# Performance work log

Hardware: AMD Instinct MI355X
Metric: run time of the kernel (lower is better)

## Reference

```python
import jax, jax.numpy as jnp
import numpy as np

B, Q, D, T, S = 64, 1024, 256, 64, 3  # batch, queries, hidden_dim, targets/image, max_steps


def _hat(w):
    # (...,3) -> (...,3,3)
    z = jnp.zeros_like(w[..., 0])
    wx, wy, wz = w[..., 0], w[..., 1], w[..., 2]
    return jnp.stack([
        jnp.stack([z, -wz, wy], -1),
        jnp.stack([wz, z, -wx], -1),
        jnp.stack([-wy, wx, z], -1),
    ], -2)


def _vee(W):
    return jnp.stack([W[..., 2, 1] - W[..., 1, 2],
                      W[..., 0, 2] - W[..., 2, 0],
                      W[..., 1, 0] - W[..., 0, 1]], -1) * 0.5


def exp_SO3(omega):
    # Rodrigues: (...,3) -> (...,3,3)
    theta = jnp.clip(jnp.linalg.norm(omega, axis=-1, keepdims=True), 1e-12, None)  # (...,1)
    K = _hat(omega / theta)
    K2 = K @ K
    I = jnp.eye(3, dtype=omega.dtype)
    st = jnp.sin(theta)[..., None]
    ct = jnp.cos(theta)[..., None]
    R = I + st * K + (1.0 - ct) * K2
    Ho = _hat(omega)
    R_small = I + Ho + 0.5 * (Ho @ Ho)
    small = (theta[..., 0] < 1e-5).astype(omega.dtype)[..., None, None]
    return R * (1.0 - small) + R_small * small


def log_SO3(R):
    # (...,3,3) -> (...,3)
    tr = jnp.clip(R[..., 0, 0] + R[..., 1, 1] + R[..., 2, 2], -1.0, 3.0)
    theta = jnp.arccos(jnp.clip((tr - 1.0) * 0.5, -1.0, 1.0))[..., None]  # (...,1)
    W = 0.5 * (R - jnp.swapaxes(R, -1, -2))
    v = _vee(W)
    w = v / jnp.clip(jnp.sin(theta), 1e-12, None) * theta
    small = (theta[..., 0] < 1e-5).astype(R.dtype)[..., None]
    return w * (1.0 - small) + v * small


def _mlp(x, w1, b1, w2, b2):
    # Linear -> ReLU -> Linear -> Sigmoid
    h = jax.nn.relu(x @ w1 + b1)
    return jax.nn.sigmoid(h @ w2 + b2)


def setup_inputs() -> dict:
    key = jax.random.key(0)
    ks = iter(jax.random.split(key, 32))

    def lin(fin, fout):
        bound = 1.0 / np.sqrt(fin)
        kw, kb = jax.random.split(next(ks))
        w = jax.random.uniform(kw, (fin, fout), jnp.float32, -bound, bound)
        b = jax.random.uniform(kb, (fout,), jnp.float32, -bound, bound)
        return w, b

    R_pred = exp_SO3(0.5 * jax.random.normal(next(ks), (B, Q, 3), jnp.float32))
    t_pred = jax.random.normal(next(ks), (B, Q, 3), jnp.float32)
    pred_boxes = jax.random.uniform(next(ks), (B, Q, 4), jnp.float32)
    query_features = jax.random.normal(next(ks), (B, Q, D), jnp.float32)
    tgt_R = exp_SO3(0.5 * jax.random.normal(next(ks), (B, T, 3), jnp.float32))
    tgt_t = jax.random.normal(next(ks), (B, T, 3), jnp.float32)
    tgt_boxes = jax.random.uniform(next(ks), (B, T, 4), jnp.float32)
    tgt_features = jax.random.normal(next(ks), (B, T, D), jnp.float32)

    sp_w1, sp_b1 = lin(D, D // 2); sp_w2, sp_b2 = lin(D // 2, S)
    rw_w1, rw_b1 = lin(D, D // 2); rw_w2, rw_b2 = lin(D // 2, 1)
    tw_w1, tw_b1 = lin(D, D // 2); tw_w2, tw_b2 = lin(D // 2, 1)
    mn_w1, mn_b1 = lin(2 * D, D);  mn_w2, mn_b2 = lin(D, 1)
    global_strength = jnp.float32(0.5)

    return dict(R_pred=R_pred, t_pred=t_pred, pred_boxes=pred_boxes,
                query_features=query_features, tgt_R=tgt_R, tgt_t=tgt_t,
                tgt_boxes=tgt_boxes, tgt_features=tgt_features,
                sp_w1=sp_w1, sp_b1=sp_b1, sp_w2=sp_w2, sp_b2=sp_b2,
                rw_w1=rw_w1, rw_b1=rw_b1, rw_w2=rw_w2, rw_b2=rw_b2,
                tw_w1=tw_w1, tw_b1=tw_b1, tw_w2=tw_w2, tw_b2=tw_b2,
                mn_w1=mn_w1, mn_b1=mn_b1, mn_w2=mn_w2, mn_b2=mn_b2,
                global_strength=global_strength)


def reference(R_pred, t_pred, pred_boxes, query_features, tgt_R, tgt_t,
              tgt_boxes, tgt_features, sp_w1, sp_b1, sp_w2, sp_b2,
              rw_w1, rw_b1, rw_w2, rw_b2, tw_w1, tw_b1, tw_w2, tw_b2,
              mn_w1, mn_b1, mn_w2, mn_b2, global_strength):
    # adaptive per-step scales: (B,S)
    step_scales = _mlp(query_features.mean(axis=1), sp_w1, sp_b1, sp_w2, sp_b2)
    step_scales = step_scales * jnp.clip(global_strength, 0.0, 1.0)
    rot_w = _mlp(query_features, rw_w1, rw_b1, rw_w2, rw_b2)    # (B,Q,1)
    trans_w = _mlp(query_features, tw_w1, tw_b1, tw_w2, tw_b2)  # (B,Q,1)

    # nearest-neighbor matching on box centers
    c_pred = pred_boxes[..., :2]               # (B,Q,2)
    cgt = tgt_boxes[..., :2]                   # (B,T,2)
    d = jnp.sum((c_pred[:, :, None, :] - cgt[:, None, :, :]) ** 2, -1)  # (B,Q,T)
    nn_idx = jnp.argmin(d, axis=-1)            # (B,Q)

    matched_feat = jnp.take_along_axis(tgt_features, nn_idx[..., None], axis=1)  # (B,Q,D)
    combined = jnp.concatenate([query_features, matched_feat], -1)               # (B,Q,2D)
    match_w = _mlp(combined, mn_w1, mn_b1, mn_w2, mn_b2)                          # (B,Q,1)

    Rmatch = jnp.take_along_axis(tgt_R, nn_idx[..., None, None], axis=1)  # (B,Q,3,3)
    tmatch = jnp.take_along_axis(tgt_t, nn_idx[..., None], axis=1)        # (B,Q,3)

    Rb, tb = R_pred, t_pred
    for s in range(S):
        scale = step_scales[:, s][:, None, None]                 # (B,1,1)
        w = log_SO3(jnp.swapaxes(Rb, -1, -2) @ Rmatch)           # (B,Q,3)
        adaptive_w = w * rot_w * match_w * scale
        Rb = Rb @ exp_SO3(adaptive_w)
        tb = tb + (tmatch - tb) * trans_w * match_w * scale
    return Rb, tb
```

## Files before the change

kernel.cpp:

```cpp
#include <hip/hip_runtime.h>

typedef __bf16 bf16;
typedef __bf16 bf16x8 __attribute__((ext_vector_type(8)));
typedef float  f32x4  __attribute__((ext_vector_type(4)));

#define QTOT 1024
#define DD   256

__global__ void k_prep(const float* __restrict__ wr, const float* __restrict__ wt,
                       const float* __restrict__ wm, const float* __restrict__ qf,
                       bf16* __restrict__ pk, float* __restrict__ wsMean2) {
  __shared__ float sPart[8][256];
  int blk = blockIdx.x;
  if (blk < 96) {
    int gid = blk * 256 + threadIdx.x;
    const float* W; int N, nK, idx; bf16* dst;
    if (gid < 4096)      { W = wr; N = 128; nK = 8;  idx = gid;        dst = pk; }
    else if (gid < 8192) { W = wt; N = 128; nK = 8;  idx = gid - 4096; dst = pk + 32768; }
    else                 { W = wm; N = 256; nK = 16; idx = gid - 8192; dst = pk + 65536; }
    int tile = idx >> 6, lane = idx & 63;
    int ni = tile / nK, ki = tile % nK;
    int l15 = lane & 15, quad = lane >> 4;
    int n = ni * 16 + l15;
    int kbase = ki * 32 + quad * 8;
    bf16x8 v;
#pragma unroll
    for (int j = 0; j < 8; ++j) v[j] = (bf16)W[(size_t)(kbase + j) * N + n];
    *(bf16x8*)(dst + (size_t)idx * 8) = v;
  } else {
    int mb = blk - 96;
    int b = mb >> 1, chunk = mb & 1;
    int tid = threadIdx.x;
    int rg = tid >> 5, c8 = tid & 31;
    float acc[8] = {0.f,0.f,0.f,0.f,0.f,0.f,0.f,0.f};
    const float* base = qf + ((size_t)b * QTOT + (size_t)chunk * 512) * DD + c8 * 8;
#pragma unroll 4
    for (int it = 0; it < 64; ++it) {
      f32x4 v0 = *(const f32x4*)(base + (size_t)(it * 8 + rg) * DD);
      f32x4 v1 = *(const f32x4*)(base + (size_t)(it * 8 + rg) * DD + 4);
#pragma unroll
      for (int j = 0; j < 4; ++j) { acc[j] += v0[j]; acc[4 + j] += v1[j]; }
    }
#pragma unroll
    for (int j = 0; j < 8; ++j) sPart[rg][c8 * 8 + j] = acc[j];
    __syncthreads();
    float s = 0.f;
#pragma unroll
    for (int g = 0; g < 8; ++g) s += sPart[g][tid];
    wsMean2[mb * 256 + tid] = s;
  }
}

__global__ void k_mid(const float* __restrict__ tgt_f, const bf16* __restrict__ pk,
                      const float* __restrict__ wsMean2,
                      const float* __restrict__ w1, const float* __restrict__ b1,
                      const float* __restrict__ w2, const float* __restrict__ b2,
                      const float* __restrict__ gs,
                      bf16* __restrict__ tgtp, float* __restrict__ outS) {
  __shared__ __align__(16) bf16 sT[64 * 264];
  __shared__ float sMean[256];
  __shared__ float sPart2[256];
  __shared__ float sHid[128];
  int blk = blockIdx.x, tid = threadIdx.x;
  if (blk < 64) {
    int b = blk;
    const float* srcT = tgt_f + ((size_t)b * 64) * DD;
#pragma unroll
    for (int it = 0; it < 8; ++it) {
      int idx = tid + it * 256;
      int row = idx >> 5, c8 = idx & 31;
      f32x4 t0 = *(const f32x4*)(srcT + (size_t)row * DD + c8 * 8);
      f32x4 t1 = *(const f32x4*)(srcT + (size_t)row * DD + c8 * 8 + 4);
      bf16x8 tv;
#pragma unroll
      for (int j = 0; j < 4; ++j) { tv[j] = (bf16)t0[j]; tv[4 + j] = (bf16)t1[j]; }
      *(bf16x8*)(sT + row * 264 + c8 * 8) = tv;
    }
    __syncthreads();
    const int lane = tid & 63, wv = tid >> 6;
    const int l15 = lane & 15, quad = lane >> 4, koff = quad * 8;
    const bf16x8* pMatch = (const bf16x8*)(pk + 65536);
    f32x4 acc[4][4];
#pragma unroll
    for (int mt = 0; mt < 4; ++mt)
#pragma unroll
      for (int nl = 0; nl < 4; ++nl) acc[mt][nl] = f32x4{0.f, 0.f, 0.f, 0.f};
#pragma unroll
    for (int ks = 0; ks < 8; ++ks) {
      bf16x8 A[4];
#pragma unroll
      for (int mt = 0; mt < 4; ++mt)
        A[mt] = *(const bf16x8*)(sT + (mt * 16 + l15) * 264 + ks * 32 + koff);
#pragma unroll
      for (int nl = 0; nl < 4; ++nl) {
        bf16x8 Bm = pMatch[((size_t)((4 * wv + nl) * 16 + 8 + ks)) * 64 + lane];
#pragma unroll
        for (int mt = 0; mt < 4; ++mt)
          acc[mt][nl] = __builtin_amdgcn_mfma_f32_16x16x32_bf16(A[mt], Bm, acc[mt][nl], 0, 0, 0);
      }
    }
    bf16* dst = tgtp + (size_t)b * 64 * 256;
#pragma unroll
    for (int mt = 0; mt < 4; ++mt)
#pragma unroll
      for (int nl = 0; nl < 4; ++nl) {
        int n = (4 * wv + nl) * 16 + l15;
#pragma unroll
        for (int i = 0; i < 4; ++i) {
          int t = mt * 16 + quad * 4 + i;
          dst[t * 256 + n] = (bf16)acc[mt][nl][i];
        }
      }
  } else {
    int b = blk - 64;
    sMean[tid] = (wsMean2[(2 * b) * 256 + tid] + wsMean2[(2 * b + 1) * 256 + tid]) * (1.f / 1024.f);
    __syncthreads();
    int hid = tid & 127, half = tid >> 7;
    float ph = 0.f;
#pragma unroll 8
    for (int dd = 0; dd < 128; ++dd) {
      int d = half * 128 + dd;
      ph += sMean[d] * w1[d * 128 + hid];
    }
    sPart2[tid] = ph;
    __syncthreads();
    if (tid < 128) sHid[tid] = fmaxf(sPart2[tid] + sPart2[tid + 128] + b1[tid], 0.f);
    __syncthreads();
    if (tid < 3) {
      float o = b2[tid];
      for (int k = 0; k < 128; ++k) o += sHid[k] * w2[k * 3 + tid];
      float g = fminf(fmaxf(gs[0], 0.f), 1.f);
      outS[b * 3 + tid] = g / (1.f + expf(-o));
    }
  }
}

__launch_bounds__(256, 4)
__global__ void k_main(const float* __restrict__ R_pred, const float* __restrict__ t_pred,
                       const float* __restrict__ pred_boxes, const float* __restrict__ qf,
                       const float* __restrict__ tgt_R, const float* __restrict__ tgt_t,
                       const float* __restrict__ tgt_boxes,
                       const float* __restrict__ rw_b1, const float* __restrict__ rw_w2, const float* __restrict__ rw_b2,
                       const float* __restrict__ tw_b1, const float* __restrict__ tw_w2, const float* __restrict__ tw_b2,
                       const float* __restrict__ mn_b1, const float* __restrict__ mn_w2, const float* __restrict__ mn_b2,
                       const bf16* __restrict__ pk, const bf16* __restrict__ tgtp,
                       const float* __restrict__ scales, float* __restrict__ out) {
  __shared__ __align__(16) bf16 sQ[64 * 264];
  __shared__ float sRedA[4][64];
  __shared__ float sRedB[4][64];
  __shared__ float sRedM[4][64];
  __shared__ int   sNN[64];

  const int tid = threadIdx.x;
  const int b  = blockIdx.x >> 4;
  const int qb = (blockIdx.x & 15) << 6;

  {
    const float* srcQ = qf + ((size_t)(b * QTOT + qb)) * DD;
#pragma unroll
    for (int it = 0; it < 8; ++it) {
      int idx = tid + it * 256;
      int row = idx >> 5, c8 = idx & 31;
      f32x4 q0 = *(const f32x4*)(srcQ + (size_t)row * DD + c8 * 8);
      f32x4 q1 = *(const f32x4*)(srcQ + (size_t)row * DD + c8 * 8 + 4);
      bf16x8 qv;
#pragma unroll
      for (int j = 0; j < 4; ++j) { qv[j] = (bf16)q0[j]; qv[4 + j] = (bf16)q1[j]; }
      *(bf16x8*)(sQ + row * 264 + c8 * 8) = qv;
    }
  }
  {
    int q = tid >> 2, ch = tid & 3;
    size_t gq = (size_t)(b * QTOT + qb + q);
    float px = pred_boxes[gq * 4 + 0];
    float py = pred_boxes[gq * 4 + 1];
    const float* tb = tgt_boxes + ((size_t)b * 64 + ch * 16) * 4;
    float best = 3.4e38f; int bi = ch * 16;
    for (int i = 0; i < 16; ++i) {
      f32x4 bx = *(const f32x4*)(tb + (size_t)i * 4);
      float dx = px - bx[0], dy = py - bx[1];
      float d = __fadd_rn(__fmul_rn(dx, dx), __fmul_rn(dy, dy));
      if (d < best) { best = d; bi = ch * 16 + i; }
    }
#pragma unroll
    for (int m = 1; m < 4; m <<= 1) {
      float pv = __shfl_xor(best, m);
      int   pi = __shfl_xor(bi, m);
      if (pv < best || (pv == best && pi < bi)) { best = pv; bi = pi; }
    }
    if ((tid & 3) == 0) sNN[q] = bi;
  }
  __syncthreads();

  const int lane = tid & 63, wv = tid >> 6;
  const int l15 = lane & 15, quad = lane >> 4;
  const int koff = quad * 8;
  const bf16x8* pRot   = (const bf16x8*)pk;
  const bf16x8* pTrans = (const bf16x8*)(pk + 32768);
  const bf16x8* pMatch = (const bf16x8*)(pk + 65536);

  {
    f32x4 accR[4][2];
#pragma unroll
    for (int mt = 0; mt < 4; ++mt)
#pragma unroll
      for (int nl = 0; nl < 2; ++nl) accR[mt][nl] = f32x4{0.f, 0.f, 0.f, 0.f};
#pragma unroll
    for (int ks = 0; ks < 8; ++ks) {
      bf16x8 A[4];
#pragma unroll
      for (int mt = 0; mt < 4; ++mt)
        A[mt] = *(const bf16x8*)(sQ + (mt * 16 + l15) * 264 + ks * 32 + koff);
#pragma unroll
      for (int nl = 0; nl < 2; ++nl) {
        bf16x8 Br = pRot[((size_t)((2 * wv + nl) * 8 + ks)) * 64 + lane];
#pragma unroll
        for (int mt = 0; mt < 4; ++mt)
          accR[mt][nl] = __builtin_amdgcn_mfma_f32_16x16x32_bf16(A[mt], Br, accR[mt][nl], 0, 0, 0);
      }
    }
    float b1r[2], w2r[2];
#pragma unroll
    for (int nl = 0; nl < 2; ++nl) {
      int n = (2 * wv + nl) * 16 + l15;
      b1r[nl] = rw_b1[n]; w2r[nl] = rw_w2[n];
    }
#pragma unroll
    for (int mt = 0; mt < 4; ++mt)
#pragma unroll
      for (int i = 0; i < 4; ++i) {
        float pr = 0.f;
#pragma unroll
        for (int nl = 0; nl < 2; ++nl) pr += fmaxf(accR[mt][nl][i] + b1r[nl], 0.f) * w2r[nl];
        pr += __shfl_xor(pr, 1); pr += __shfl_xor(pr, 2); pr += __shfl_xor(pr, 4); pr += __shfl_xor(pr, 8);
        if (l15 == 0) sRedA[wv][mt * 16 + quad * 4 + i] = pr;
      }
  }
  {
    f32x4 accT[4][2];
#pragma unroll
    for (int mt = 0; mt < 4; ++mt)
#pragma unroll
      for (int nl = 0; nl < 2; ++nl) accT[mt][nl] = f32x4{0.f, 0.f, 0.f, 0.f};
#pragma unroll
    for (int ks = 0; ks < 8; ++ks) {
      bf16x8 A[4];
#pragma unroll
      for (int mt = 0; mt < 4; ++mt)
        A[mt] = *(const bf16x8*)(sQ + (mt * 16 + l15) * 264 + ks * 32 + koff);
#pragma unroll
      for (int nl = 0; nl < 2; ++nl) {
        bf16x8 Bt = pTrans[((size_t)((2 * wv + nl) * 8 + ks)) * 64 + lane];
#pragma unroll
        for (int mt = 0; mt < 4; ++mt)
          accT[mt][nl] = __builtin_amdgcn_mfma_f32_16x16x32_bf16(A[mt], Bt, accT[mt][nl], 0, 0, 0);
      }
    }
    float b1t[2], w2t[2];
#pragma unroll
    for (int nl = 0; nl < 2; ++nl) {
      int n = (2 * wv + nl) * 16 + l15;
      b1t[nl] = tw_b1[n]; w2t[nl] = tw_w2[n];
    }
#pragma unroll
    for (int mt = 0; mt < 4; ++mt)
#pragma unroll
      for (int i = 0; i < 4; ++i) {
        float pt = 0.f;
#pragma unroll
        for (int nl = 0; nl < 2; ++nl) pt += fmaxf(accT[mt][nl][i] + b1t[nl], 0.f) * w2t[nl];
        pt += __shfl_xor(pt, 1); pt += __shfl_xor(pt, 2); pt += __shfl_xor(pt, 4); pt += __shfl_xor(pt, 8);
        if (l15 == 0) sRedB[wv][mt * 16 + quad * 4 + i] = pt;
      }
  }
  __syncthreads();

  float rw, tw;
  {
    int q = wv * 16 + l15;
    float vr = sRedA[0][q] + sRedA[1][q] + sRedA[2][q] + sRedA[3][q] + rw_b2[0];
    float vt = sRedB[0][q] + sRedB[1][q] + sRedB[2][q] + sRedB[3][q] + tw_b2[0];
    rw = 1.f / (1.f + expf(-vr));
    tw = 1.f / (1.f + expf(-vt));
  }

  {
    f32x4 accM[4][4];
#pragma unroll
    for (int mt = 0; mt < 4; ++mt)
#pragma unroll
      for (int nl = 0; nl < 4; ++nl) accM[mt][nl] = f32x4{0.f, 0.f, 0.f, 0.f};
#pragma unroll
    for (int ks = 0; ks < 8; ++ks) {
      bf16x8 A[4];
#pragma unroll
      for (int mt = 0; mt < 4; ++mt)
        A[mt] = *(const bf16x8*)(sQ + (mt * 16 + l15) * 264 + ks * 32 + koff);
#pragma unroll
      for (int nl = 0; nl < 4; ++nl) {
        bf16x8 Bm = pMatch[((size_t)((4 * wv + nl) * 16 + ks)) * 64 + lane];
#pragma unroll
        for (int mt = 0; mt < 4; ++mt)
          accM[mt][nl] = __builtin_amdgcn_mfma_f32_16x16x32_bf16(A[mt], Bm, accM[mt][nl], 0, 0, 0);
      }
    }
    float b1m[4], w2m[4];
#pragma unroll
    for (int nl = 0; nl < 4; ++nl) {
      int n = (4 * wv + nl) * 16 + l15;
      b1m[nl] = mn_b1[n]; w2m[nl] = mn_w2[n];
    }
    const bf16* tpb = tgtp + (size_t)b * 64 * 256;
#pragma unroll
    for (int mt = 0; mt < 4; ++mt)
#pragma unroll
      for (int i = 0; i < 4; ++i) {
        int nnq = sNN[mt * 16 + quad * 4 + i];
        const bf16* tprow = tpb + (size_t)nnq * 256;
        float pm = 0.f;
#pragma unroll
        for (int nl = 0; nl < 4; ++nl) {
          float tp = (float)tprow[(4 * wv + nl) * 16 + l15];
          pm += fmaxf(accM[mt][nl][i] + b1m[nl] + tp, 0.f) * w2m[nl];
        }
        pm += __shfl_xor(pm, 1); pm += __shfl_xor(pm, 2); pm += __shfl_xor(pm, 4); pm += __shfl_xor(pm, 8);
        if (l15 == 0) sRedM[wv][mt * 16 + quad * 4 + i] = pm;
      }
  }
  __syncthreads();

  if (quad == 0) {
    int q = wv * 16 + l15;
    float vm = sRedM[0][q] + sRedM[1][q] + sRedM[2][q] + sRedM[3][q] + mn_b2[0];
    float mw = 1.f / (1.f + expf(-vm));
    size_t gq = (size_t)(b * QTOT + qb + q);
    float R[9], Rm[9], t[3], tm[3];
#pragma unroll
    for (int i = 0; i < 9; ++i) R[i] = R_pred[gq * 9 + i];
#pragma unroll
    for (int c = 0; c < 3; ++c) t[c] = t_pred[gq * 3 + c];
    size_t gt = (size_t)b * 64 + sNN[q];
#pragma unroll
    for (int i = 0; i < 9; ++i) Rm[i] = tgt_R[gt * 9 + i];
#pragma unroll
    for (int c = 0; c < 3; ++c) tm[c] = tgt_t[gt * 3 + c];

    for (int s = 0; s < 3; ++s) {
      float sc = scales[b * 3 + s];
      float cr = rw * mw * sc, ctr = tw * mw * sc;
      float Ax[9];
#pragma unroll
      for (int i = 0; i < 3; ++i)
#pragma unroll
        for (int j = 0; j < 3; ++j)
          Ax[i * 3 + j] = R[0 + i] * Rm[0 + j] + R[3 + i] * Rm[3 + j] + R[6 + i] * Rm[6 + j];
      float tr = fminf(fmaxf(Ax[0] + Ax[4] + Ax[8], -1.f), 3.f);
      float cthe = fminf(fmaxf((tr - 1.f) * 0.5f, -1.f), 1.f);
      float th = acosf(cthe);
      float vx = 0.5f * (Ax[7] - Ax[5]);
      float vy = 0.5f * (Ax[2] - Ax[6]);
      float vz = 0.5f * (Ax[3] - Ax[1]);
      float f = (th < 1e-5f) ? 1.f : th / fmaxf(sinf(th), 1e-12f);
      float ax = vx * f * cr, ay = vy * f * cr, az = vz * f * cr;
      float th2 = ax * ax + ay * ay + az * az;
      float thn = sqrtf(th2);
      float E[9];
      if (thn < 1e-5f) {
        E[0] = 1.f + 0.5f * (ax * ax - th2); E[1] = -az + 0.5f * ax * ay;        E[2] =  ay + 0.5f * ax * az;
        E[3] =  az + 0.5f * ax * ay;         E[4] = 1.f + 0.5f * (ay * ay - th2); E[5] = -ax + 0.5f * ay * az;
        E[6] = -ay + 0.5f * ax * az;         E[7] =  ax + 0.5f * ay * az;         E[8] = 1.f + 0.5f * (az * az - th2);
      } else {
        float kx = ax / thn, ky = ay / thn, kz = az / thn;
        float st = sinf(thn), co = cosf(thn), c1 = 1.f - co;
        E[0] = co + c1 * kx * kx;      E[1] = c1 * kx * ky - st * kz; E[2] = c1 * kx * kz + st * ky;
        E[3] = c1 * kx * ky + st * kz; E[4] = co + c1 * ky * ky;      E[5] = c1 * ky * kz - st * kx;
        E[6] = c1 * kx * kz - st * ky; E[7] = c1 * ky * kz + st * kx; E[8] = co + c1 * kz * kz;
      }
      float Rn[9];
#pragma unroll
      for (int i = 0; i < 3; ++i)
#pragma unroll
        for (int j = 0; j < 3; ++j)
          Rn[i * 3 + j] = R[i * 3 + 0] * E[j] + R[i * 3 + 1] * E[3 + j] + R[i * 3 + 2] * E[6 + j];
#pragma unroll
      for (int i = 0; i < 9; ++i) R[i] = Rn[i];
#pragma unroll
      for (int c = 0; c < 3; ++c) t[c] += (tm[c] - t[c]) * ctr;
    }
#pragma unroll
    for (int i = 0; i < 9; ++i) out[gq * 9 + i] = R[i];
#pragma unroll
    for (int c = 0; c < 3; ++c) out[(size_t)589824 + gq * 3 + c] = t[c];
  }
}

extern "C" void kernel_launch(void* const* d_in, const int* in_sizes, int n_in,
                              void* d_out, int out_size, void* d_ws, size_t ws_size,
                              hipStream_t stream) {
  const float* R_pred     = (const float*)d_in[0];
  const float* t_pred     = (const float*)d_in[1];
  const float* pred_boxes = (const float*)d_in[2];
  const float* qf         = (const float*)d_in[3];
  const float* tgt_R      = (const float*)d_in[4];
  const float* tgt_t      = (const float*)d_in[5];
  const float* tgt_boxes  = (const float*)d_in[6];
  const float* tgt_f      = (const float*)d_in[7];
  const float* sp_w1 = (const float*)d_in[8];
  const float* sp_b1 = (const float*)d_in[9];
  const float* sp_w2 = (const float*)d_in[10];
  const float* sp_b2 = (const float*)d_in[11];
  const float* rw_w1 = (const float*)d_in[12];
  const float* rw_b1 = (const float*)d_in[13];
  const float* rw_w2 = (const float*)d_in[14];
  const float* rw_b2 = (const float*)d_in[15];
  const float* tw_w1 = (const float*)d_in[16];
  const float* tw_b1 = (const float*)d_in[17];
  const float* tw_w2 = (const float*)d_in[18];
  const float* tw_b2 = (const float*)d_in[19];
  const float* mn_w1 = (const float*)d_in[20];
  const float* mn_b1 = (const float*)d_in[21];
  const float* mn_w2 = (const float*)d_in[22];
  const float* mn_b2 = (const float*)d_in[23];
  const float* gs    = (const float*)d_in[24];

  float* wsScales = (float*)d_ws;
  float* wsMean2  = (float*)((char*)d_ws + 1024);
  bf16*  pk       = (bf16*)((char*)d_ws + 1024 + 131072);
  bf16*  tgtp     = (bf16*)((char*)d_ws + 1024 + 131072 + 393216);
  float* out      = (float*)d_out;

  k_prep<<<224, 256, 0, stream>>>(rw_w1, tw_w1, mn_w1, qf, pk, wsMean2);
  k_mid<<<128, 256, 0, stream>>>(tgt_f, pk, wsMean2, sp_w1, sp_b1, sp_w2, sp_b2, gs, tgtp, wsScales);
  k_main<<<1024, 256, 0, stream>>>(R_pred, t_pred, pred_boxes, qf, tgt_R, tgt_t, tgt_boxes,
                                   rw_b1, rw_w2, rw_b2, tw_b1, tw_w2, tw_b2, mn_b1, mn_w2, mn_b2,
                                   pk, tgtp, wsScales, out);
}
```

Before: 212.5 us.

## Give each wave its own 16 queries, keep A fragments in registers, drop LDS

Splits work so each wave owns 16 queries and computes all hidden units of the three MLPs for them, instead of all four waves splitting the hidden units of 64 shared queries. Query features are loaded from global straight into register A fragments, which removes the shared sQ tile, the cross-wave partial-sum reductions and the block-level barriers. In exchange, every wave now streams the full packed weight matrices, which multiplies weight loads per block by four. Register pressure also rises from holding eight A fragments.

```diff
diff --git a/kernel.cpp b/kernel.cpp
--- a/kernel.cpp
+++ b/kernel.cpp
@@ -145,33 +145,18 @@
                        const float* __restrict__ mn_b1, const float* __restrict__ mn_w2, const float* __restrict__ mn_b2,
                        const bf16* __restrict__ pk, const bf16* __restrict__ tgtp,
                        const float* __restrict__ scales, float* __restrict__ out) {
-  __shared__ __align__(16) bf16 sQ[64 * 264];
-  __shared__ float sRedA[4][64];
-  __shared__ float sRedB[4][64];
-  __shared__ float sRedM[4][64];
-  __shared__ int   sNN[64];
+  __shared__ float sRW[4][16], sTW[4][16], sMW[4][16];
+  __shared__ int   sNNw[4][16];
 
   const int tid = threadIdx.x;
+  const int lane = tid & 63, wv = tid >> 6;
+  const int l15 = lane & 15, quad = lane >> 4;
   const int b  = blockIdx.x >> 4;
-  const int qb = (blockIdx.x & 15) << 6;
-
-  {
-    const float* srcQ = qf + ((size_t)(b * QTOT + qb)) * DD;
-#pragma unroll
-    for (int it = 0; it < 8; ++it) {
-      int idx = tid + it * 256;
-      int row = idx >> 5, c8 = idx & 31;
-      f32x4 q0 = *(const f32x4*)(srcQ + (size_t)row * DD + c8 * 8);
-      f32x4 q1 = *(const f32x4*)(srcQ + (size_t)row * DD + c8 * 8 + 4);
-      bf16x8 qv;
-#pragma unroll
-      for (int j = 0; j < 4; ++j) { qv[j] = (bf16)q0[j]; qv[4 + j] = (bf16)q1[j]; }
-      *(bf16x8*)(sQ + row * 264 + c8 * 8) = qv;
-    }
-  }
-  {
-    int q = tid >> 2, ch = tid & 3;
-    size_t gq = (size_t)(b * QTOT + qb + q);
+  const int qw = ((blockIdx.x & 15) << 6) + wv * 16;
+
+  {
+    int q = lane >> 2, ch = lane & 3;
+    size_t gq = (size_t)(b * QTOT + qw + q);
     float px = pred_boxes[gq * 4 + 0];
     float py = pred_boxes[gq * 4 + 1];
     const float* tb = tgt_boxes + ((size_t)b * 64 + ch * 16) * 4;
@@ -188,158 +173,131 @@
       int   pi = __shfl_xor(bi, m);
       if (pv < best || (pv == best && pi < bi)) { best = pv; bi = pi; }
     }
-    if ((tid & 3) == 0) sNN[q] = bi;
-  }
-  __syncthreads();
-
-  const int lane = tid & 63, wv = tid >> 6;
-  const int l15 = lane & 15, quad = lane >> 4;
-  const int koff = quad * 8;
+    if (ch == 0) sNNw[wv][q] = bi;
+  }
+
+  bf16x8 Areg[8];
+  {
+    const float* rowp = qf + ((size_t)(b * QTOT + qw + l15)) * DD + quad * 8;
+#pragma unroll
+    for (int ks = 0; ks < 8; ++ks) {
+      f32x4 a0 = *(const f32x4*)(rowp + ks * 32);
+      f32x4 a1 = *(const f32x4*)(rowp + ks * 32 + 4);
+#pragma unroll
+      for (int j = 0; j < 4; ++j) { Areg[ks][j] = (bf16)a0[j]; Areg[ks][4 + j] = (bf16)a1[j]; }
+    }
+  }
+
   const bf16x8* pRot   = (const bf16x8*)pk;
   const bf16x8* pTrans = (const bf16x8*)(pk + 32768);
   const bf16x8* pMatch = (const bf16x8*)(pk + 65536);
 
   {
-    f32x4 accR[4][2];
-#pragma unroll
-    for (int mt = 0; mt < 4; ++mt)
-#pragma unroll
-      for (int nl = 0; nl < 2; ++nl) accR[mt][nl] = f32x4{0.f, 0.f, 0.f, 0.f};
-#pragma unroll
-    for (int ks = 0; ks < 8; ++ks) {
-      bf16x8 A[4];
-#pragma unroll
-      for (int mt = 0; mt < 4; ++mt)
-        A[mt] = *(const bf16x8*)(sQ + (mt * 16 + l15) * 264 + ks * 32 + koff);
-#pragma unroll
-      for (int nl = 0; nl < 2; ++nl) {
-        bf16x8 Br = pRot[((size_t)((2 * wv + nl) * 8 + ks)) * 64 + lane];
-#pragma unroll
-        for (int mt = 0; mt < 4; ++mt)
-          accR[mt][nl] = __builtin_amdgcn_mfma_f32_16x16x32_bf16(A[mt], Br, accR[mt][nl], 0, 0, 0);
-      }
-    }
-    float b1r[2], w2r[2];
-#pragma unroll
-    for (int nl = 0; nl < 2; ++nl) {
-      int n = (2 * wv + nl) * 16 + l15;
-      b1r[nl] = rw_b1[n]; w2r[nl] = rw_w2[n];
-    }
-#pragma unroll
-    for (int mt = 0; mt < 4; ++mt)
-#pragma unroll
-      for (int i = 0; i < 4; ++i) {
-        float pr = 0.f;
-#pragma unroll
-        for (int nl = 0; nl < 2; ++nl) pr += fmaxf(accR[mt][nl][i] + b1r[nl], 0.f) * w2r[nl];
-        pr += __shfl_xor(pr, 1); pr += __shfl_xor(pr, 2); pr += __shfl_xor(pr, 4); pr += __shfl_xor(pr, 8);
-        if (l15 == 0) sRedA[wv][mt * 16 + quad * 4 + i] = pr;
-      }
-  }
-  {
-    f32x4 accT[4][2];
-#pragma unroll
-    for (int mt = 0; mt < 4; ++mt)
-#pragma unroll
-      for (int nl = 0; nl < 2; ++nl) accT[mt][nl] = f32x4{0.f, 0.f, 0.f, 0.f};
-#pragma unroll
-    for (int ks = 0; ks < 8; ++ks) {
-      bf16x8 A[4];
-#pragma unroll
-      for (int mt = 0; mt < 4; ++mt)
-        A[mt] = *(const bf16x8*)(sQ + (mt * 16 + l15) * 264 + ks * 32 + koff);
-#pragma unroll
-      for (int nl = 0; nl < 2; ++nl) {
-        bf16x8 Bt = pTrans[((size_t)((2 * wv + nl) * 8 + ks)) * 64 + lane];
-#pragma unroll
-        for (int mt = 0; mt < 4; ++mt)
-          accT[mt][nl] = __builtin_amdgcn_mfma_f32_16x16x32_bf16(A[mt], Bt, accT[mt][nl], 0, 0, 0);
-      }
-    }
-    float b1t[2], w2t[2];
-#pragma unroll
-    for (int nl = 0; nl < 2; ++nl) {
-      int n = (2 * wv + nl) * 16 + l15;
-      b1t[nl] = tw_b1[n]; w2t[nl] = tw_w2[n];
-    }
-#pragma unroll
-    for (int mt = 0; mt < 4; ++mt)
-#pragma unroll
-      for (int i = 0; i < 4; ++i) {
-        float pt = 0.f;
-#pragma unroll
-        for (int nl = 0; nl < 2; ++nl) pt += fmaxf(accT[mt][nl][i] + b1t[nl], 0.f) * w2t[nl];
-        pt += __shfl_xor(pt, 1); pt += __shfl_xor(pt, 2); pt += __shfl_xor(pt, 4); pt += __shfl_xor(pt, 8);
-        if (l15 == 0) sRedB[wv][mt * 16 + quad * 4 + i] = pt;
-      }
-  }
-  __syncthreads();
-
-  float rw, tw;
-  {
-    int q = wv * 16 + l15;
-    float vr = sRedA[0][q] + sRedA[1][q] + sRedA[2][q] + sRedA[3][q] + rw_b2[0];
-    float vt = sRedB[0][q] + sRedB[1][q] + sRedB[2][q] + sRedB[3][q] + tw_b2[0];
-    rw = 1.f / (1.f + expf(-vr));
-    tw = 1.f / (1.f + expf(-vt));
-  }
-
-  {
-    f32x4 accM[4][4];
-#pragma unroll
-    for (int mt = 0; mt < 4; ++mt)
-#pragma unroll
-      for (int nl = 0; nl < 4; ++nl) accM[mt][nl] = f32x4{0.f, 0.f, 0.f, 0.f};
-#pragma unroll
-    for (int ks = 0; ks < 8; ++ks) {
-      bf16x8 A[4];
-#pragma unroll
-      for (int mt = 0; mt < 4; ++mt)
-        A[mt] = *(const bf16x8*)(sQ + (mt * 16 + l15) * 264 + ks * 32 + koff);
-#pragma unroll
-      for (int nl = 0; nl < 4; ++nl) {
-        bf16x8 Bm = pMatch[((size_t)((4 * wv + nl) * 16 + ks)) * 64 + lane];
-#pragma unroll
-        for (int mt = 0; mt < 4; ++mt)
-          accM[mt][nl] = __builtin_amdgcn_mfma_f32_16x16x32_bf16(A[mt], Bm, accM[mt][nl], 0, 0, 0);
-      }
-    }
-    float b1m[4], w2m[4];
-#pragma unroll
-    for (int nl = 0; nl < 4; ++nl) {
-      int n = (4 * wv + nl) * 16 + l15;
-      b1m[nl] = mn_b1[n]; w2m[nl] = mn_w2[n];
-    }
+    float pm[4] = {0.f, 0.f, 0.f, 0.f};
+#pragma unroll
+    for (int c = 0; c < 2; ++c) {
+      f32x4 acc[4];
+#pragma unroll
+      for (int nl = 0; nl < 4; ++nl) acc[nl] = f32x4{0.f, 0.f, 0.f, 0.f};
+#pragma unroll
+      for (int ks = 0; ks < 8; ++ks)
+#pragma unroll
+        for (int nl = 0; nl < 4; ++nl)
+          acc[nl] = __builtin_amdgcn_mfma_f32_16x16x32_bf16(
+              Areg[ks], pRot[((c * 4 + nl) * 8 + ks) * 64 + lane], acc[nl], 0, 0, 0);
+#pragma unroll
+      for (int nl = 0; nl < 4; ++nl) {
+        int n = (c * 4 + nl) * 16 + l15;
+        float b1 = rw_b1[n], w2 = rw_w2[n];
+#pragma unroll
+        for (int i = 0; i < 4; ++i) pm[i] += fmaxf(acc[nl][i] + b1, 0.f) * w2;
+      }
+    }
+#pragma unroll
+    for (int i = 0; i < 4; ++i) {
+      float v = pm[i];
+      v += __shfl_xor(v, 1); v += __shfl_xor(v, 2); v += __shfl_xor(v, 4); v += __shfl_xor(v, 8);
+      if (l15 == 0) sRW[wv][quad * 4 + i] = v;
+    }
+  }
+  {
+    float pm[4] = {0.f, 0.f, 0.f, 0.f};
+#pragma unroll
+    for (int c = 0; c < 2; ++c) {
+      f32x4 acc[4];
+#pragma unroll
+      for (int nl = 0; nl < 4; ++nl) acc[nl] = f32x4{0.f, 0.f, 0.f, 0.f};
+#pragma unroll
+      for (int ks = 0; ks < 8; ++ks)
+#pragma unroll
+        for (int nl = 0; nl < 4; ++nl)
+          acc[nl] = __builtin_amdgcn_mfma_f32_16x16x32_bf16(
+              Areg[ks], pTrans[((c * 4 + nl) * 8 + ks) * 64 + lane], acc[nl], 0, 0, 0);
+#pragma unroll
+      for (int nl = 0; nl < 4; ++nl) {
+        int n = (c * 4 + nl) * 16 + l15;
+        float b1 = tw_b1[n], w2 = tw_w2[n];
+#pragma unroll
+        for (int i = 0; i < 4; ++i) pm[i] += fmaxf(acc[nl][i] + b1, 0.f) * w2;
+      }
+    }
+#pragma unroll
+    for (int i = 0; i < 4; ++i) {
+      float v = pm[i];
+      v += __shfl_xor(v, 1); v += __shfl_xor(v, 2); v += __shfl_xor(v, 4); v += __shfl_xor(v, 8);
+      if (l15 == 0) sTW[wv][quad * 4 + i] = v;
+    }
+  }
+  {
+    float pm[4] = {0.f, 0.f, 0.f, 0.f};
     const bf16* tpb = tgtp + (size_t)b * 64 * 256;
-#pragma unroll
-    for (int mt = 0; mt < 4; ++mt)
-#pragma unroll
-      for (int i = 0; i < 4; ++i) {
-        int nnq = sNN[mt * 16 + quad * 4 + i];
-        const bf16* tprow = tpb + (size_t)nnq * 256;
-        float pm = 0.f;
-#pragma unroll
-        for (int nl = 0; nl < 4; ++nl) {
-          float tp = (float)tprow[(4 * wv + nl) * 16 + l15];
-          pm += fmaxf(accM[mt][nl][i] + b1m[nl] + tp, 0.f) * w2m[nl];
+    int nn_i[4];
+#pragma unroll
+    for (int i = 0; i < 4; ++i) nn_i[i] = sNNw[wv][quad * 4 + i];
+#pragma unroll
+    for (int c = 0; c < 4; ++c) {
+      f32x4 acc[4];
+#pragma unroll
+      for (int nl = 0; nl < 4; ++nl) acc[nl] = f32x4{0.f, 0.f, 0.f, 0.f};
+#pragma unroll
+      for (int ks = 0; ks < 8; ++ks)
+#pragma unroll
+        for (int nl = 0; nl < 4; ++nl)
+          acc[nl] = __builtin_amdgcn_mfma_f32_16x16x32_bf16(
+              Areg[ks], pMatch[((c * 4 + nl) * 16 + ks) * 64 + lane], acc[nl], 0, 0, 0);
+#pragma unroll
+      for (int nl = 0; nl < 4; ++nl) {
+        int n = (c * 4 + nl) * 16 + l15;
+        float b1 = mn_b1[n], w2 = mn_w2[n];
+#pragma unroll
+        for (int i = 0; i < 4; ++i) {
+          float tp = (float)tpb[(size_t)nn_i[i] * 256 + n];
+          pm[i] += fmaxf(acc[nl][i] + b1 + tp, 0.f) * w2;
         }
-        pm += __shfl_xor(pm, 1); pm += __shfl_xor(pm, 2); pm += __shfl_xor(pm, 4); pm += __shfl_xor(pm, 8);
-        if (l15 == 0) sRedM[wv][mt * 16 + quad * 4 + i] = pm;
-      }
-  }
-  __syncthreads();
+      }
+    }
+#pragma unroll
+    for (int i = 0; i < 4; ++i) {
+      float v = pm[i];
+      v += __shfl_xor(v, 1); v += __shfl_xor(v, 2); v += __shfl_xor(v, 4); v += __shfl_xor(v, 8);
+      if (l15 == 0) sMW[wv][quad * 4 + i] = v;
+    }
+  }
+
+  __builtin_amdgcn_wave_barrier();
 
   if (quad == 0) {
-    int q = wv * 16 + l15;
-    float vm = sRedM[0][q] + sRedM[1][q] + sRedM[2][q] + sRedM[3][q] + mn_b2[0];
-    float mw = 1.f / (1.f + expf(-vm));
-    size_t gq = (size_t)(b * QTOT + qb + q);
+    int q = l15;
+    float rw = 1.f / (1.f + expf(-(sRW[wv][q] + rw_b2[0])));
+    float tw = 1.f / (1.f + expf(-(sTW[wv][q] + tw_b2[0])));
+    float mw = 1.f / (1.f + expf(-(sMW[wv][q] + mn_b2[0])));
+    size_t gq = (size_t)(b * QTOT + qw + q);
     float R[9], Rm[9], t[3], tm[3];
 #pragma unroll
     for (int i = 0; i < 9; ++i) R[i] = R_pred[gq * 9 + i];
 #pragma unroll
     for (int c = 0; c < 3; ++c) t[c] = t_pred[gq * 3 + c];
-    size_t gt = (size_t)b * 64 + sNN[q];
+    size_t gt = (size_t)b * 64 + sNNw[wv][q];
 #pragma unroll
     for (int i = 0; i < 9; ++i) Rm[i] = tgt_R[gt * 9 + i];
 #pragma unroll
```

New measurement: 267.2 us. 25.8% more time.

## Write bf16 query copy in prep and split SO3 refinement into separate kernel

Applied to the files above, without the earlier changes.

The prep kernel, which already reads all query features to compute means, now also writes a bf16 copy when the workspace is large enough. The main kernel then loads half the bytes per tile. The per-query SO3 refinement loop moves out of the MFMA kernel into a new fully parallel kernel that reads sigmoid weights and the nn index from a workspace buffer. Previously that loop ran on only a quarter of each block's threads. The split adds an extra kernel launch, a 32 MB bf16 write plus its re-read, and a dependence on workspace size.

```diff
diff --git a/kernel.cpp b/kernel.cpp
--- a/kernel.cpp
+++ b/kernel.cpp
@@ -9,7 +9,8 @@
 
 __global__ void k_prep(const float* __restrict__ wr, const float* __restrict__ wt,
                        const float* __restrict__ wm, const float* __restrict__ qf,
-                       bf16* __restrict__ pk, float* __restrict__ wsMean2) {
+                       bf16* __restrict__ pk, float* __restrict__ wsMean2,
+                       bf16* __restrict__ qf16, int useQ16) {
   __shared__ float sPart[8][256];
   int blk = blockIdx.x;
   if (blk < 96) {
@@ -33,13 +34,20 @@
     int tid = threadIdx.x;
     int rg = tid >> 5, c8 = tid & 31;
     float acc[8] = {0.f,0.f,0.f,0.f,0.f,0.f,0.f,0.f};
-    const float* base = qf + ((size_t)b * QTOT + (size_t)chunk * 512) * DD + c8 * 8;
-#pragma unroll 4
+#pragma unroll 2
     for (int it = 0; it < 64; ++it) {
-      f32x4 v0 = *(const f32x4*)(base + (size_t)(it * 8 + rg) * DD);
-      f32x4 v1 = *(const f32x4*)(base + (size_t)(it * 8 + rg) * DD + 4);
+      int row = chunk * 512 + it * 8 + rg;
+      const float* rp = qf + ((size_t)b * QTOT + row) * DD + c8 * 8;
+      f32x4 v0 = *(const f32x4*)rp;
+      f32x4 v1 = *(const f32x4*)(rp + 4);
 #pragma unroll
       for (int j = 0; j < 4; ++j) { acc[j] += v0[j]; acc[4 + j] += v1[j]; }
+      if (useQ16) {
+        bf16x8 qv;
+#pragma unroll
+        for (int j = 0; j < 4; ++j) { qv[j] = (bf16)v0[j]; qv[4 + j] = (bf16)v1[j]; }
+        *(bf16x8*)(qf16 + ((size_t)b * QTOT + row) * DD + c8 * 8) = qv;
+      }
     }
 #pragma unroll
     for (int j = 0; j < 8; ++j) sPart[rg][c8 * 8 + j] = acc[j];
@@ -136,15 +144,14 @@
 }
 
 __launch_bounds__(256, 4)
-__global__ void k_main(const float* __restrict__ R_pred, const float* __restrict__ t_pred,
-                       const float* __restrict__ pred_boxes, const float* __restrict__ qf,
-                       const float* __restrict__ tgt_R, const float* __restrict__ tgt_t,
+__global__ void k_main(const float* __restrict__ pred_boxes, const float* __restrict__ qf,
+                       const bf16* __restrict__ qf16, int useQ16,
                        const float* __restrict__ tgt_boxes,
                        const float* __restrict__ rw_b1, const float* __restrict__ rw_w2, const float* __restrict__ rw_b2,
                        const float* __restrict__ tw_b1, const float* __restrict__ tw_w2, const float* __restrict__ tw_b2,
                        const float* __restrict__ mn_b1, const float* __restrict__ mn_w2, const float* __restrict__ mn_b2,
                        const bf16* __restrict__ pk, const bf16* __restrict__ tgtp,
-                       const float* __restrict__ scales, float* __restrict__ out) {
+                       f32x4* __restrict__ wsW) {
   __shared__ __align__(16) bf16 sQ[64 * 264];
   __shared__ float sRedA[4][64];
   __shared__ float sRedB[4][64];
@@ -155,7 +162,15 @@
   const int b  = blockIdx.x >> 4;
   const int qb = (blockIdx.x & 15) << 6;
 
-  {
+  if (useQ16) {
+    const bf16* srcQ = qf16 + ((size_t)(b * QTOT + qb)) * DD;
+#pragma unroll
+    for (int it = 0; it < 8; ++it) {
+      int idx = tid + it * 256;
+      int row = idx >> 5, c8 = idx & 31;
+      *(bf16x8*)(sQ + row * 264 + c8 * 8) = *(const bf16x8*)(srcQ + (size_t)row * DD + c8 * 8);
+    }
+  } else {
     const float* srcQ = qf + ((size_t)(b * QTOT + qb)) * DD;
 #pragma unroll
     for (int it = 0; it < 8; ++it) {
@@ -213,7 +228,7 @@
         A[mt] = *(const bf16x8*)(sQ + (mt * 16 + l15) * 264 + ks * 32 + koff);
 #pragma unroll
       for (int nl = 0; nl < 2; ++nl) {
-        bf16x8 Br = pRot[((size_t)((2 * wv + nl) * 8 + ks)) * 64 + lane];
+        bf16x8 Br = pRot[((2 * wv + nl) * 8 + ks) * 64 + lane];
 #pragma unroll
         for (int mt = 0; mt < 4; ++mt)
           accR[mt][nl] = __builtin_amdgcn_mfma_f32_16x16x32_bf16(A[mt], Br, accR[mt][nl], 0, 0, 0);
@@ -250,7 +265,7 @@
         A[mt] = *(const bf16x8*)(sQ + (mt * 16 + l15) * 264 + ks * 32 + koff);
 #pragma unroll
       for (int nl = 0; nl < 2; ++nl) {
-        bf16x8 Bt = pTrans[((size_t)((2 * wv + nl) * 8 + ks)) * 64 + lane];
+        bf16x8 Bt = pTrans[((2 * wv + nl) * 8 + ks) * 64 + lane];
 #pragma unroll
         for (int mt = 0; mt < 4; ++mt)
           accT[mt][nl] = __builtin_amdgcn_mfma_f32_16x16x32_bf16(A[mt], Bt, accT[mt][nl], 0, 0, 0);
@@ -273,17 +288,6 @@
         if (l15 == 0) sRedB[wv][mt * 16 + quad * 4 + i] = pt;
       }
   }
-  __syncthreads();
-
-  float rw, tw;
-  {
-    int q = wv * 16 + l15;
-    float vr = sRedA[0][q] + sRedA[1][q] + sRedA[2][q] + sRedA[3][q] + rw_b2[0];
-    float vt = sRedB[0][q] + sRedB[1][q] + sRedB[2][q] + sRedB[3][q] + tw_b2[0];
-    rw = 1.f / (1.f + expf(-vr));
-    tw = 1.f / (1.f + expf(-vt));
-  }
-
   {
     f32x4 accM[4][4];
 #pragma unroll
@@ -298,7 +302,7 @@
         A[mt] = *(const bf16x8*)(sQ + (mt * 16 + l15) * 264 + ks * 32 + koff);
 #pragma unroll
       for (int nl = 0; nl < 4; ++nl) {
-        bf16x8 Bm = pMatch[((size_t)((4 * wv + nl) * 16 + ks)) * 64 + lane];
+        bf16x8 Bm = pMatch[((4 * wv + nl) * 16 + ks) * 64 + lane];
 #pragma unroll
         for (int mt = 0; mt < 4; ++mt)
           accM[mt][nl] = __builtin_amdgcn_mfma_f32_16x16x32_bf16(A[mt], Bm, accM[mt][nl], 0, 0, 0);
@@ -329,69 +333,86 @@
   }
   __syncthreads();
 
-  if (quad == 0) {
-    int q = wv * 16 + l15;
+  if (tid < 64) {
+    int q = tid;
+    float vr = sRedA[0][q] + sRedA[1][q] + sRedA[2][q] + sRedA[3][q] + rw_b2[0];
+    float vt = sRedB[0][q] + sRedB[1][q] + sRedB[2][q] + sRedB[3][q] + tw_b2[0];
     float vm = sRedM[0][q] + sRedM[1][q] + sRedM[2][q] + sRedM[3][q] + mn_b2[0];
-    float mw = 1.f / (1.f + expf(-vm));
-    size_t gq = (size_t)(b * QTOT + qb + q);
-    float R[9], Rm[9], t[3], tm[3];
-#pragma unroll
-    for (int i = 0; i < 9; ++i) R[i] = R_pred[gq * 9 + i];
-#pragma unroll
-    for (int c = 0; c < 3; ++c) t[c] = t_pred[gq * 3 + c];
-    size_t gt = (size_t)b * 64 + sNN[q];
-#pragma unroll
-    for (int i = 0; i < 9; ++i) Rm[i] = tgt_R[gt * 9 + i];
-#pragma unroll
-    for (int c = 0; c < 3; ++c) tm[c] = tgt_t[gt * 3 + c];
-
-    for (int s = 0; s < 3; ++s) {
-      float sc = scales[b * 3 + s];
-      float cr = rw * mw * sc, ctr = tw * mw * sc;
-      float Ax[9];
-#pragma unroll
-      for (int i = 0; i < 3; ++i)
-#pragma unroll
-        for (int j = 0; j < 3; ++j)
-          Ax[i * 3 + j] = R[0 + i] * Rm[0 + j] + R[3 + i] * Rm[3 + j] + R[6 + i] * Rm[6 + j];
-      float tr = fminf(fmaxf(Ax[0] + Ax[4] + Ax[8], -1.f), 3.f);
-      float cthe = fminf(fmaxf((tr - 1.f) * 0.5f, -1.f), 1.f);
-      float th = acosf(cthe);
-      float vx = 0.5f * (Ax[7] - Ax[5]);
-      float vy = 0.5f * (Ax[2] - Ax[6]);
-      float vz = 0.5f * (Ax[3] - Ax[1]);
-      float f = (th < 1e-5f) ? 1.f : th / fmaxf(sinf(th), 1e-12f);
-      float ax = vx * f * cr, ay = vy * f * cr, az = vz * f * cr;
-      float th2 = ax * ax + ay * ay + az * az;
-      float thn = sqrtf(th2);
-      float E[9];
-      if (thn < 1e-5f) {
-        E[0] = 1.f + 0.5f * (ax * ax - th2); E[1] = -az + 0.5f * ax * ay;        E[2] =  ay + 0.5f * ax * az;
-        E[3] =  az + 0.5f * ax * ay;         E[4] = 1.f + 0.5f * (ay * ay - th2); E[5] = -ax + 0.5f * ay * az;
-        E[6] = -ay + 0.5f * ax * az;         E[7] =  ax + 0.5f * ay * az;         E[8] = 1.f + 0.5f * (az * az - th2);
-      } else {
-        float kx = ax / thn, ky = ay / thn, kz = az / thn;
-        float st = sinf(thn), co = cosf(thn), c1 = 1.f - co;
-        E[0] = co + c1 * kx * kx;      E[1] = c1 * kx * ky - st * kz; E[2] = c1 * kx * kz + st * ky;
-        E[3] = c1 * kx * ky + st * kz; E[4] = co + c1 * ky * ky;      E[5] = c1 * ky * kz - st * kx;
-        E[6] = c1 * kx * kz - st * ky; E[7] = c1 * ky * kz + st * kx; E[8] = co + c1 * kz * kz;
-      }
-      float Rn[9];
-#pragma unroll
-      for (int i = 0; i < 3; ++i)
-#pragma unroll
-        for (int j = 0; j < 3; ++j)
-          Rn[i * 3 + j] = R[i * 3 + 0] * E[j] + R[i * 3 + 1] * E[3 + j] + R[i * 3 + 2] * E[6 + j];
-#pragma unroll
-      for (int i = 0; i < 9; ++i) R[i] = Rn[i];
-#pragma unroll
-      for (int c = 0; c < 3; ++c) t[c] += (tm[c] - t[c]) * ctr;
-    }
-#pragma unroll
-    for (int i = 0; i < 9; ++i) out[gq * 9 + i] = R[i];
-#pragma unroll
-    for (int c = 0; c < 3; ++c) out[(size_t)589824 + gq * 3 + c] = t[c];
-  }
+    f32x4 w;
+    w[0] = 1.f / (1.f + expf(-vr));
+    w[1] = 1.f / (1.f + expf(-vt));
+    w[2] = 1.f / (1.f + expf(-vm));
+    w[3] = __int_as_float(sNN[q]);
+    wsW[(size_t)(b * QTOT + qb + q)] = w;
+  }
+}
+
+__global__ void k_so3(const float* __restrict__ R_pred, const float* __restrict__ t_pred,
+                      const float* __restrict__ tgt_R, const float* __restrict__ tgt_t,
+                      const f32x4* __restrict__ wsW, const float* __restrict__ scales,
+                      float* __restrict__ out) {
+  int gq = blockIdx.x * 256 + threadIdx.x;
+  int b = gq >> 10;
+  f32x4 w = wsW[gq];
+  float rw = w[0], tw = w[1], mw = w[2];
+  int nn = __float_as_int(w[3]);
+  float R[9], Rm[9], t[3], tm[3];
+#pragma unroll
+  for (int i = 0; i < 9; ++i) R[i] = R_pred[(size_t)gq * 9 + i];
+#pragma unroll
+  for (int c = 0; c < 3; ++c) t[c] = t_pred[(size_t)gq * 3 + c];
+  size_t gt = (size_t)b * 64 + nn;
+#pragma unroll
+  for (int i = 0; i < 9; ++i) Rm[i] = tgt_R[gt * 9 + i];
+#pragma unroll
+  for (int c = 0; c < 3; ++c) tm[c] = tgt_t[gt * 3 + c];
+
+  for (int s = 0; s < 3; ++s) {
+    float sc = scales[b * 3 + s];
+    float cr = rw * mw * sc, ctr = tw * mw * sc;
+    float Ax[9];
+#pragma unroll
+    for (int i = 0; i < 3; ++i)
+#pragma unroll
+      for (int j = 0; j < 3; ++j)
+        Ax[i * 3 + j] = R[0 + i] * Rm[0 + j] + R[3 + i] * Rm[3 + j] + R[6 + i] * Rm[6 + j];
+    float tr = fminf(fmaxf(Ax[0] + Ax[4] + Ax[8], -1.f), 3.f);
+    float cthe = fminf(fmaxf((tr - 1.f) * 0.5f, -1.f), 1.f);
+    float th = acosf(cthe);
+    float vx = 0.5f * (Ax[7] - Ax[5]);
+    float vy = 0.5f * (Ax[2] - Ax[6]);
+    float vz = 0.5f * (Ax[3] - Ax[1]);
+    float f = (th < 1e-5f) ? 1.f : th / fmaxf(sinf(th), 1e-12f);
+    float ax = vx * f * cr, ay = vy * f * cr, az = vz * f * cr;
+    float th2 = ax * ax + ay * ay + az * az;
+    float thn = sqrtf(th2);
+    float E[9];
+    if (thn < 1e-5f) {
+      E[0] = 1.f + 0.5f * (ax * ax - th2); E[1] = -az + 0.5f * ax * ay;        E[2] =  ay + 0.5f * ax * az;
+      E[3] =  az + 0.5f * ax * ay;         E[4] = 1.f + 0.5f * (ay * ay - th2); E[5] = -ax + 0.5f * ay * az;
+      E[6] = -ay + 0.5f * ax * az;         E[7] =  ax + 0.5f * ay * az;         E[8] = 1.f + 0.5f * (az * az - th2);
+    } else {
+      float kx = ax / thn, ky = ay / thn, kz = az / thn;
+      float st = sinf(thn), co = cosf(thn), c1 = 1.f - co;
+      E[0] = co + c1 * kx * kx;      E[1] = c1 * kx * ky - st * kz; E[2] = c1 * kx * kz + st * ky;
+      E[3] = c1 * kx * ky + st * kz; E[4] = co + c1 * ky * ky;      E[5] = c1 * ky * kz - st * kx;
+      E[6] = c1 * kx * kz - st * ky; E[7] = c1 * ky * kz + st * kx; E[8] = co + c1 * kz * kz;
+    }
+    float Rn[9];
+#pragma unroll
+    for (int i = 0; i < 3; ++i)
+#pragma unroll
+      for (int j = 0; j < 3; ++j)
+        Rn[i * 3 + j] = R[i * 3 + 0] * E[j] + R[i * 3 + 1] * E[3 + j] + R[i * 3 + 2] * E[6 + j];
+#pragma unroll
+    for (int i = 0; i < 9; ++i) R[i] = Rn[i];
+#pragma unroll
+    for (int c = 0; c < 3; ++c) t[c] += (tm[c] - t[c]) * ctr;
+  }
+#pragma unroll
+  for (int i = 0; i < 9; ++i) out[(size_t)gq * 9 + i] = R[i];
+#pragma unroll
+  for (int c = 0; c < 3; ++c) out[(size_t)589824 + (size_t)gq * 3 + c] = t[c];
 }
 
 extern "C" void kernel_launch(void* const* d_in, const int* in_sizes, int n_in,
@@ -423,15 +444,21 @@
   const float* mn_b2 = (const float*)d_in[23];
   const float* gs    = (const float*)d_in[24];
 
-  float* wsScales = (float*)d_ws;
-  float* wsMean2  = (float*)((char*)d_ws + 1024);
-  bf16*  pk       = (bf16*)((char*)d_ws + 1024 + 131072);
-  bf16*  tgtp     = (bf16*)((char*)d_ws + 1024 + 131072 + 393216);
+  char* ws = (char*)d_ws;
+  float* wsScales = (float*)ws;
+  float* wsMean2  = (float*)(ws + 1024);
+  bf16*  pk       = (bf16*)(ws + 1024 + 131072);
+  bf16*  tgtp     = (bf16*)(ws + 1024 + 131072 + 393216);
+  f32x4* wsW      = (f32x4*)(ws + 1024 + 131072 + 393216 + 2097152);
+  bf16*  qf16     = (bf16*)(ws + 1024 + 131072 + 393216 + 2097152 + 1048576);
+  size_t need16   = 1024 + 131072 + 393216 + 2097152 + 1048576 + (size_t)QTOT * 64 * DD * 2;
+  int useQ16      = (ws_size >= need16) ? 1 : 0;
   float* out      = (float*)d_out;
 
-  k_prep<<<224, 256, 0, stream>>>(rw_w1, tw_w1, mn_w1, qf, pk, wsMean2);
+  k_prep<<<224, 256, 0, stream>>>(rw_w1, tw_w1, mn_w1, qf, pk, wsMean2, qf16, useQ16);
   k_mid<<<128, 256, 0, stream>>>(tgt_f, pk, wsMean2, sp_w1, sp_b1, sp_w2, sp_b2, gs, tgtp, wsScales);
-  k_main<<<1024, 256, 0, stream>>>(R_pred, t_pred, pred_boxes, qf, tgt_R, tgt_t, tgt_boxes,
+  k_main<<<1024, 256, 0, stream>>>(pred_boxes, qf, qf16, useQ16, tgt_boxes,
                                    rw_b1, rw_w2, rw_b2, tw_b1, tw_w2, tw_b2, mn_b1, mn_w2, mn_b2,
-                                   pk, tgtp, wsScales, out);
+                                   pk, tgtp, wsW);
+  k_so3<<<256, 256, 0, stream>>>(R_pred, t_pred, tgt_R, tgt_t, wsW, wsScales, out);
 }
```

Result: slower. 252.8 us (+19.0%).
